# Kernel optimization log

Measured on AMD Instinct MI355X. Metric: run time of the kernel, lower is better.

## Reference

```python
import jax, jax.numpy as jnp
import numpy as np

BETA = 0.25
NUM_EMBEDS = 1024
EMBED_DIM = 256


def setup_inputs() -> dict:
    key = jax.random.key(0)
    k1, k2 = jax.random.split(key)
    z_e = jax.random.normal(k1, (32, EMBED_DIM, 1024), dtype=jnp.float32)
    lim = 1.0 / NUM_EMBEDS
    embed_weight = jax.random.uniform(k2, (NUM_EMBEDS, EMBED_DIM), dtype=jnp.float32,
                                      minval=-lim, maxval=lim)
    return {"z_e": z_e, "embed_weight": embed_weight}


def reference(z_e, embed_weight):
    # z_e: (b, d, t) -> (b, t, d)
    ze = jnp.transpose(z_e, (0, 2, 1))
    b, t, d = ze.shape
    flat = ze.reshape(-1, d)  # (N, d)
    K = embed_weight.shape[0]
    # squared euclidean distances (N, K) via sum-of-squares + matmul
    distances = (jnp.sum(flat ** 2, axis=1, keepdims=True)
                 + jnp.sum(embed_weight ** 2, axis=1)
                 - 2.0 * flat @ embed_weight.T)
    idx = jnp.argmin(distances, axis=1)  # (N,)
    # one-hot @ W is just a gather
    z_q = embed_weight[idx].reshape(b, t, d)
    # commitment / codebook losses (mse over all elements)
    e_latent_loss = jnp.mean((jax.lax.stop_gradient(z_q) - ze) ** 2)
    q_latent_loss = jnp.mean((z_q - jax.lax.stop_gradient(ze)) ** 2)
    reg_loss = q_latent_loss + BETA * e_latent_loss
    # straight-through estimator
    z_q_st = ze + jax.lax.stop_gradient(z_q - ze)
    z_q_out = jnp.transpose(z_q_st, (0, 2, 1))  # (b, d, t)
    # perplexity from codebook usage
    N = flat.shape[0]
    avg_probs = jnp.zeros((K,), dtype=jnp.float32).at[idx].add(1.0) / N
    perplexity = jnp.exp(-jnp.sum(avg_probs * jnp.log(avg_probs + 1e-10)))
    return (z_q_out, reg_loss, perplexity)
```

## Files before the change

kernel.cpp:

```cpp
#include <hip/hip_runtime.h>
#include <math.h>

#define BB 32
#define DD 256
#define TT 1024
#define KK 1024
#define NN (BB*TT)

#define BROWS 64
#define CCH   256
#define DSL   64
#define NSTEP 16


__global__ void prep_kernel(const float* __restrict__ W, float* __restrict__ wsq,
                            int* __restrict__ counts, float* __restrict__ sse) {
    const int k = blockIdx.x;
    const int lane = threadIdx.x;
    const float4 v = ((const float4*)(W + (size_t)k * DD))[lane];
    double s = (double)v.x * v.x + (double)v.y * v.y + (double)v.z * v.z + (double)v.w * v.w;
    #pragma unroll
    for (int m = 32; m > 0; m >>= 1) s += __shfl_down(s, m);
    if (lane == 0) wsq[k] = (float)s;
    if (blockIdx.x < 16) counts[blockIdx.x * 64 + lane] = 0;
    if (blockIdx.x == 0 && lane == 0) *sse = 0.0f;
}

__device__ __forceinline__ int swz_w(int r, int q) { return r * 16 + (q ^ ((r >> 3) & 7)); }
__device__ __forceinline__ int swz_z(int r, int q) { return r * 16 + (q ^ (r & 7) ^ ((r >> 3) & 7)); }

__device__ __forceinline__ void gl_lds16(const float* g, void* l) {
    __builtin_amdgcn_global_load_lds((const __attribute__((address_space(1))) void*)g,
                                     (__attribute__((address_space(3))) void*)l, 16, 0, 0);
}

__global__ __launch_bounds__(256, 2) void vq_fused_kernel(
    const float* __restrict__ z, const float* __restrict__ W,
    const float* __restrict__ wsq, float* __restrict__ out,
    int* __restrict__ counts, float* __restrict__ sse)
{
    __shared__ float4 zs[BROWS * 16];
    __shared__ float4 ws[CCH * 16];
    const int tid = threadIdx.x;
    const int tx = tid & 31, ty = tid >> 5;
    const int w = tid >> 6, lane = tid & 63;
    const int row0 = blockIdx.x * BROWS;
    const int b = row0 >> 10, t0 = row0 & 1023;
    const size_t bbase = (size_t)b * DD * TT;
    const float* zbase = z + bbase + t0;

    float rsq[8];
    {
        const int ro = lane & 15;
        const int g  = lane >> 4;
        const float* zp = zbase + (size_t)g * 64 * TT + (16 * w + ro);
        double s = 0.0;
        #pragma unroll 4
        for (int d = 0; d < 64; ++d) { float v = zp[(size_t)d * TT]; s += (double)v * v; }
        s += __shfl_xor(s, 16);
        s += __shfl_xor(s, 32);
        float f = (float)s;
        #pragma unroll
        for (int i = 0; i < 8; ++i) rsq[i] = __shfl(f, (ty & 1) * 8 + i);
    }

    float minv[8]; int mini[8];
    #pragma unroll
    for (int i = 0; i < 8; ++i) { minv[i] = 3.4e38f; mini[i] = 0; }

    const int zr = tid & 63;
    const int zq0 = w * 4;
    float4 zreg[4];
    {
        #pragma unroll
        for (int j = 0; j < 4; ++j) {
            const float* zp = zbase + (size_t)((zq0 + j) * 4) * TT + zr;
            zreg[j].x = zp[0]; zreg[j].y = zp[(size_t)TT];
            zreg[j].z = zp[(size_t)2 * TT]; zreg[j].w = zp[(size_t)3 * TT];
        }
    }

    const int wr0 = w * 64 + (lane >> 4);
    const int wslot = lane & 15;
    char* const wlbase = (char*)ws + (size_t)w * 16384;

    float acc[8][8];
    float wq[8];

    for (int s = 0; s < NSTEP; ++s) {
        const int sl = s & 3, ch = s >> 2;
        __syncthreads();
        #pragma unroll
        for (int j = 0; j < 4; ++j) zs[swz_z(zr, zq0 + j)] = zreg[j];
        {
            const float* wch = W + (size_t)(ch * CCH) * DD + sl * DSL;
            #pragma unroll
            for (int k = 0; k < 16; ++k) {
                int r = wr0 + k * 4;
                const float* g = wch + (size_t)r * DD + 4 * (wslot ^ ((r >> 3) & 7));
                gl_lds16(g, wlbase + k * 1024);
            }
        }
        __syncthreads();

        if (sl == 0) {
            #pragma unroll
            for (int i = 0; i < 8; ++i)
                #pragma unroll
                for (int j = 0; j < 8; ++j) acc[i][j] = 0.0f;
            #pragma unroll
            for (int j = 0; j < 8; ++j) wq[j] = wsq[ch * CCH + tx * 8 + j];
        }
        if (s < NSTEP - 1) {
            const int sln = (s + 1) & 3;
            #pragma unroll
            for (int j = 0; j < 4; ++j) {
                const float* zp = zbase + (size_t)(sln * DSL + (zq0 + j) * 4) * TT + zr;
                zreg[j].x = zp[0]; zreg[j].y = zp[(size_t)TT];
                zreg[j].z = zp[(size_t)2 * TT]; zreg[j].w = zp[(size_t)3 * TT];
            }
        }
        for (int q = 0; q < 16; ++q) {
            float4 zf[8], wf[8];
            #pragma unroll
            for (int i = 0; i < 8; ++i) zf[i] = zs[swz_z(ty * 8 + i, q)];
            #pragma unroll
            for (int j = 0; j < 8; ++j) wf[j] = ws[swz_w(tx * 8 + j, q)];
            #pragma unroll
            for (int i = 0; i < 8; ++i)
                #pragma unroll
                for (int j = 0; j < 8; ++j) {
                    acc[i][j] = fmaf(zf[i].x, wf[j].x, acc[i][j]);
                    acc[i][j] = fmaf(zf[i].y, wf[j].y, acc[i][j]);
                    acc[i][j] = fmaf(zf[i].z, wf[j].z, acc[i][j]);
                    acc[i][j] = fmaf(zf[i].w, wf[j].w, acc[i][j]);
                }
        }
        if (sl == 3) {
            #pragma unroll
            for (int j = 0; j < 8; ++j) {
                int c = ch * CCH + tx * 8 + j;
                #pragma unroll
                for (int i = 0; i < 8; ++i) {
                    float s1 = rsq[i] + wq[j];
                    float v = fmaf(-2.0f, acc[i][j], s1);
                    if (v < minv[i]) { minv[i] = v; mini[i] = c; }
                }
            }
        }
    }

    __syncthreads();
    int* idxs = (int*)zs;
    float* ssescr = (float*)zs + 64;
    #pragma unroll
    for (int i = 0; i < 8; ++i) {
        float v = minv[i]; int ix = mini[i];
        #pragma unroll
        for (int m = 1; m < 32; m <<= 1) {
            float ov = __shfl_xor(v, m);
            int   oi = __shfl_xor(ix, m);
            if (ov < v || (ov == v && oi < ix)) { v = ov; ix = oi; }
        }
        if (tx == 0) {
            idxs[ty * 8 + i] = ix;
            atomicAdd(&counts[ix], 1);
        }
    }
    __syncthreads();

    const int tg = tid & 15;
    const int dg = tid >> 4;
    const int t4 = tg * 4;
    int ixs[4];
    #pragma unroll
    for (int m = 0; m < 4; ++m) ixs[m] = idxs[t4 + m];
    float ssel = 0.0f;
    #pragma unroll
    for (int k4 = 0; k4 < 4; ++k4) {
        const int d0 = dg * 16 + k4 * 4;
        float wr[4][4];
        #pragma unroll
        for (int m = 0; m < 4; ++m) {
            float4 wv = *(const float4*)(W + (size_t)ixs[m] * DD + d0);
            wr[m][0] = wv.x; wr[m][1] = wv.y; wr[m][2] = wv.z; wr[m][3] = wv.w;
        }
        #pragma unroll
        for (int dd = 0; dd < 4; ++dd) {
            const int d = d0 + dd;
            const size_t base = bbase + (size_t)d * TT + t0 + t4;
            float4 zv = *(const float4*)(z + base);
            float e0 = wr[0][dd] - zv.x, e1 = wr[1][dd] - zv.y;
            float e2 = wr[2][dd] - zv.z, e3 = wr[3][dd] - zv.w;
            float4 o;
            o.x = zv.x + e0; o.y = zv.y + e1; o.z = zv.z + e2; o.w = zv.w + e3;
            *(float4*)(out + base) = o;
            ssel += (e0 * e0 + e1 * e1) + (e2 * e2 + e3 * e3);
        }
    }
    #pragma unroll
    for (int m = 32; m > 0; m >>= 1) ssel += __shfl_down(ssel, m);
    if (lane == 0) ssescr[w] = ssel;
    __syncthreads();
    if (tid == 0) atomicAdd(sse, (ssescr[0] + ssescr[1]) + (ssescr[2] + ssescr[3]));
}

__global__ void finalize_kernel(const int* __restrict__ counts, const float* __restrict__ sse,
                                float* __restrict__ out) {
    float s = 0.0f;
    for (int k = threadIdx.x; k < KK; k += 256) {
        float p = (float)counts[k] / (float)NN;
        s += p * logf(p + 1e-10f);
    }
    #pragma unroll
    for (int m = 32; m > 0; m >>= 1) s += __shfl_down(s, m);
    __shared__ float wsum[4];
    if ((threadIdx.x & 63) == 0) wsum[threadIdx.x >> 6] = s;
    __syncthreads();
    if (threadIdx.x == 0) {
        float ent = (wsum[0] + wsum[1]) + (wsum[2] + wsum[3]);
        out[(size_t)BB * DD * TT]     = 1.25f * (*sse) / (float)(BB * DD * TT);
        out[(size_t)BB * DD * TT + 1] = expf(-ent);
    }
}

extern "C" void kernel_launch(void* const* d_in, const int* in_sizes, int n_in,
                              void* d_out, int out_size, void* d_ws, size_t ws_size,
                              hipStream_t stream) {
    const float* z = (const float*)d_in[0];
    const float* W = (const float*)d_in[1];
    float* out = (float*)d_out;

    float* wsq    = (float*)d_ws;
    int*   counts = (int*)(wsq + 1024);
    float* sse    = (float*)(counts + 1024);

    prep_kernel<<<1024, 64, 0, stream>>>(W, wsq, counts, sse);
    vq_fused_kernel<<<NN / BROWS, 256, 0, stream>>>(z, W, wsq, out, counts, sse);
    finalize_kernel<<<1, 256, 0, stream>>>(counts, sse, out);
}
```

Before: 272.2 us.

## Double-buffer LDS tiles with one barrier per step and a narrower K slice

Splits the shared-memory z and W tiles into two buffers. The next step's tiles (W via global_load_lds, z from registers) are staged while the current buffer is being computed, so each step needs one barrier instead of two. The K slice per step shrinks from 64 to 32 dims (32 steps instead of 16), which keeps total LDS the same. The inner q loop is now fully unrolled. This is meant to hide global-to-LDS latency behind the FMA work, at the cost of twice as many barriers across steps, larger code, and more register pressure.

```diff
diff --git a/kernel.cpp b/kernel.cpp
--- a/kernel.cpp
+++ b/kernel.cpp
@@ -9,8 +9,8 @@
 
 #define BROWS 64
 #define CCH   256
-#define DSL   64
-#define NSTEP 16
+#define DSL   32
+#define NSTEP 32
 
 
 __global__ void prep_kernel(const float* __restrict__ W, float* __restrict__ wsq,
@@ -26,8 +26,8 @@
     if (blockIdx.x == 0 && lane == 0) *sse = 0.0f;
 }
 
-__device__ __forceinline__ int swz_w(int r, int q) { return r * 16 + (q ^ ((r >> 3) & 7)); }
-__device__ __forceinline__ int swz_z(int r, int q) { return r * 16 + (q ^ (r & 7) ^ ((r >> 3) & 7)); }
+__device__ __forceinline__ int swz_w(int r, int q) { return r * 8 + (q ^ ((r >> 3) & 7)); }
+__device__ __forceinline__ int swz_z(int r, int q) { return r * 8 + (q ^ (r & 7) ^ ((r >> 3) & 7)); }
 
 __device__ __forceinline__ void gl_lds16(const float* g, void* l) {
     __builtin_amdgcn_global_load_lds((const __attribute__((address_space(1))) void*)g,
@@ -39,8 +39,8 @@
     const float* __restrict__ wsq, float* __restrict__ out,
     int* __restrict__ counts, float* __restrict__ sse)
 {
-    __shared__ float4 zs[BROWS * 16];
-    __shared__ float4 ws[CCH * 16];
+    __shared__ float4 zs[2][BROWS * 8];
+    __shared__ float4 ws[2][CCH * 8];
     const int tid = threadIdx.x;
     const int tx = tid & 31, ty = tid >> 5;
     const int w = tid >> 6, lane = tid & 63;
@@ -68,41 +68,53 @@
     #pragma unroll
     for (int i = 0; i < 8; ++i) { minv[i] = 3.4e38f; mini[i] = 0; }
 
-    const int zr = tid & 63;
-    const int zq0 = w * 4;
-    float4 zreg[4];
-    {
-        #pragma unroll
-        for (int j = 0; j < 4; ++j) {
-            const float* zp = zbase + (size_t)((zq0 + j) * 4) * TT + zr;
+    const int zr  = lane;
+    const int zq0 = w * 2;
+    const int wlr = lane >> 3;
+    const int wls = lane & 7;
+    float4 zreg[2];
+
+    auto STAGE_W = [&](int t) {
+        const int ch = t >> 3, sl = t & 7;
+        const float* wch = W + (size_t)(ch * CCH) * DD + sl * DSL;
+        char* dst = (char*)&ws[t & 1][0] + (size_t)w * 8192;
+        #pragma unroll
+        for (int k = 0; k < 8; ++k) {
+            const int r = w * 64 + k * 8 + wlr;
+            const float* g = wch + (size_t)r * DD + 4 * (wls ^ k);
+            gl_lds16(g, dst + k * 1024);
+        }
+    };
+    auto LOAD_Z = [&](int t) {
+        const int sl = t & 7;
+        #pragma unroll
+        for (int j = 0; j < 2; ++j) {
+            const float* zp = zbase + (size_t)(sl * DSL + (zq0 + j) * 4) * TT + zr;
             zreg[j].x = zp[0]; zreg[j].y = zp[(size_t)TT];
             zreg[j].z = zp[(size_t)2 * TT]; zreg[j].w = zp[(size_t)3 * TT];
         }
-    }
-
-    const int wr0 = w * 64 + (lane >> 4);
-    const int wslot = lane & 15;
-    char* const wlbase = (char*)ws + (size_t)w * 16384;
+    };
+    auto WRITE_Z = [&](int t) {
+        #pragma unroll
+        for (int j = 0; j < 2; ++j) zs[t & 1][swz_z(zr, zq0 + j)] = zreg[j];
+    };
+
+    LOAD_Z(0);
+    STAGE_W(0);
+    WRITE_Z(0);
+    LOAD_Z(1);
 
     float acc[8][8];
     float wq[8];
 
     for (int s = 0; s < NSTEP; ++s) {
-        const int sl = s & 3, ch = s >> 2;
+        const int sl = s & 7, ch = s >> 3;
         __syncthreads();
-        #pragma unroll
-        for (int j = 0; j < 4; ++j) zs[swz_z(zr, zq0 + j)] = zreg[j];
-        {
-            const float* wch = W + (size_t)(ch * CCH) * DD + sl * DSL;
-            #pragma unroll
-            for (int k = 0; k < 16; ++k) {
-                int r = wr0 + k * 4;
-                const float* g = wch + (size_t)r * DD + 4 * (wslot ^ ((r >> 3) & 7));
-                gl_lds16(g, wlbase + k * 1024);
-            }
-        }
-        __syncthreads();
-
+        if (s + 1 < NSTEP) {
+            STAGE_W(s + 1);
+            WRITE_Z(s + 1);
+            if (s + 2 < NSTEP) LOAD_Z(s + 2);
+        }
         if (sl == 0) {
             #pragma unroll
             for (int i = 0; i < 8; ++i)
@@ -111,21 +123,13 @@
             #pragma unroll
             for (int j = 0; j < 8; ++j) wq[j] = wsq[ch * CCH + tx * 8 + j];
         }
-        if (s < NSTEP - 1) {
-            const int sln = (s + 1) & 3;
-            #pragma unroll
-            for (int j = 0; j < 4; ++j) {
-                const float* zp = zbase + (size_t)(sln * DSL + (zq0 + j) * 4) * TT + zr;
-                zreg[j].x = zp[0]; zreg[j].y = zp[(size_t)TT];
-                zreg[j].z = zp[(size_t)2 * TT]; zreg[j].w = zp[(size_t)3 * TT];
-            }
-        }
-        for (int q = 0; q < 16; ++q) {
+        #pragma unroll
+        for (int q = 0; q < 8; ++q) {
             float4 zf[8], wf[8];
             #pragma unroll
-            for (int i = 0; i < 8; ++i) zf[i] = zs[swz_z(ty * 8 + i, q)];
-            #pragma unroll
-            for (int j = 0; j < 8; ++j) wf[j] = ws[swz_w(tx * 8 + j, q)];
+            for (int i = 0; i < 8; ++i) zf[i] = zs[s & 1][swz_z(ty * 8 + i, q)];
+            #pragma unroll
+            for (int j = 0; j < 8; ++j) wf[j] = ws[s & 1][swz_w(tx * 8 + j, q)];
             #pragma unroll
             for (int i = 0; i < 8; ++i)
                 #pragma unroll
@@ -136,7 +140,7 @@
                     acc[i][j] = fmaf(zf[i].w, wf[j].w, acc[i][j]);
                 }
         }
-        if (sl == 3) {
+        if (sl == 7) {
             #pragma unroll
             for (int j = 0; j < 8; ++j) {
                 int c = ch * CCH + tx * 8 + j;
@@ -151,8 +155,8 @@
     }
 
     __syncthreads();
-    int* idxs = (int*)zs;
-    float* ssescr = (float*)zs + 64;
+    int* idxs = (int*)&zs[0][0];
+    float* ssescr = (float*)&zs[0][0] + 64;
     #pragma unroll
     for (int i = 0; i < 8; ++i) {
         float v = minv[i]; int ix = mini[i];
```

Measured after the change: 408.3 us. 1.5x slower.

## Double-buffer codebook tiles in LDS with async prefetch of next slice

Applied to the files above, without the earlier changes.

The codebook LDS tile is split into two half-size buffers (32-wide d-slices) so the global-to-LDS load for the next step is issued before computing on the current one. The z tile is still written once per 64-wide slice and consumed over two steps. This is meant to hide W load latency behind the FMA loop instead of stalling on a barrier after each load. The cost is twice as many steps and barriers, with LDS size unchanged.

```diff
diff --git a/kernel.cpp b/kernel.cpp
--- a/kernel.cpp
+++ b/kernel.cpp
@@ -9,8 +9,8 @@
 
 #define BROWS 64
 #define CCH   256
-#define DSL   64
-#define NSTEP 16
+#define WSL   32
+#define NSTEP 32
 
 
 __global__ void prep_kernel(const float* __restrict__ W, float* __restrict__ wsq,
@@ -26,8 +26,8 @@
     if (blockIdx.x == 0 && lane == 0) *sse = 0.0f;
 }
 
-__device__ __forceinline__ int swz_w(int r, int q) { return r * 16 + (q ^ ((r >> 3) & 7)); }
 __device__ __forceinline__ int swz_z(int r, int q) { return r * 16 + (q ^ (r & 7) ^ ((r >> 3) & 7)); }
+__device__ __forceinline__ int swz_w(int r, int q) { return r * 8 + (q ^ ((r >> 3) & 7)); }
 
 __device__ __forceinline__ void gl_lds16(const float* g, void* l) {
     __builtin_amdgcn_global_load_lds((const __attribute__((address_space(1))) void*)g,
@@ -40,7 +40,7 @@
     int* __restrict__ counts, float* __restrict__ sse)
 {
     __shared__ float4 zs[BROWS * 16];
-    __shared__ float4 ws[CCH * 16];
+    __shared__ float4 ws[2][CCH * 8];
     const int tid = threadIdx.x;
     const int tx = tid & 31, ty = tid >> 5;
     const int w = tid >> 6, lane = tid & 63;
@@ -48,6 +48,28 @@
     const int b = row0 >> 10, t0 = row0 & 1023;
     const size_t bbase = (size_t)b * DD * TT;
     const float* zbase = z + bbase + t0;
+
+    const int zr  = lane;
+    const int zq0 = w * 4;
+    const int wlr = lane >> 3;
+    const int wls = lane & 7;
+    float4 zreg[4];
+
+    {
+        const float* wch = W;
+        char* dst = (char*)&ws[0][0] + (size_t)w * 8192;
+        #pragma unroll
+        for (int k = 0; k < 8; ++k) {
+            const int r = w * 64 + k * 8 + wlr;
+            gl_lds16(wch + (size_t)r * DD + 4 * (wls ^ k), dst + k * 1024);
+        }
+        #pragma unroll
+        for (int j = 0; j < 4; ++j) {
+            const float* zp = zbase + (size_t)((zq0 + j) * 4) * TT + zr;
+            zreg[j].x = zp[0]; zreg[j].y = zp[(size_t)TT];
+            zreg[j].z = zp[(size_t)2 * TT]; zreg[j].w = zp[(size_t)3 * TT];
+        }
+    }
 
     float rsq[8];
     {
@@ -68,41 +90,36 @@
     #pragma unroll
     for (int i = 0; i < 8; ++i) { minv[i] = 3.4e38f; mini[i] = 0; }
 
-    const int zr = tid & 63;
-    const int zq0 = w * 4;
-    float4 zreg[4];
-    {
-        #pragma unroll
-        for (int j = 0; j < 4; ++j) {
-            const float* zp = zbase + (size_t)((zq0 + j) * 4) * TT + zr;
-            zreg[j].x = zp[0]; zreg[j].y = zp[(size_t)TT];
-            zreg[j].z = zp[(size_t)2 * TT]; zreg[j].w = zp[(size_t)3 * TT];
-        }
-    }
-
-    const int wr0 = w * 64 + (lane >> 4);
-    const int wslot = lane & 15;
-    char* const wlbase = (char*)ws + (size_t)w * 16384;
-
     float acc[8][8];
     float wq[8];
 
     for (int s = 0; s < NSTEP; ++s) {
-        const int sl = s & 3, ch = s >> 2;
+        const int h = s & 1, sl = s & 7, ch = s >> 3;
         __syncthreads();
-        #pragma unroll
-        for (int j = 0; j < 4; ++j) zs[swz_z(zr, zq0 + j)] = zreg[j];
-        {
-            const float* wch = W + (size_t)(ch * CCH) * DD + sl * DSL;
-            #pragma unroll
-            for (int k = 0; k < 16; ++k) {
-                int r = wr0 + k * 4;
-                const float* g = wch + (size_t)r * DD + 4 * (wslot ^ ((r >> 3) & 7));
-                gl_lds16(g, wlbase + k * 1024);
+        if (h == 0) {
+            #pragma unroll
+            for (int j = 0; j < 4; ++j) zs[swz_z(zr, zq0 + j)] = zreg[j];
+            __syncthreads();
+        }
+        if (s + 1 < NSTEP) {
+            const int t = s + 1, sln = t & 7, chn = t >> 3;
+            const float* wch = W + (size_t)(chn * CCH) * DD + sln * WSL;
+            char* dst = (char*)&ws[t & 1][0] + (size_t)w * 8192;
+            #pragma unroll
+            for (int k = 0; k < 8; ++k) {
+                const int r = w * 64 + k * 8 + wlr;
+                gl_lds16(wch + (size_t)r * DD + 4 * (wls ^ k), dst + k * 1024);
             }
         }
-        __syncthreads();
-
+        if (h == 0 && s + 2 < NSTEP) {
+            const int mn = ((s + 2) & 7) >> 1;
+            #pragma unroll
+            for (int j = 0; j < 4; ++j) {
+                const float* zp = zbase + (size_t)(mn * 64 + (zq0 + j) * 4) * TT + zr;
+                zreg[j].x = zp[0]; zreg[j].y = zp[(size_t)TT];
+                zreg[j].z = zp[(size_t)2 * TT]; zreg[j].w = zp[(size_t)3 * TT];
+            }
+        }
         if (sl == 0) {
             #pragma unroll
             for (int i = 0; i < 8; ++i)
@@ -111,21 +128,13 @@
             #pragma unroll
             for (int j = 0; j < 8; ++j) wq[j] = wsq[ch * CCH + tx * 8 + j];
         }
-        if (s < NSTEP - 1) {
-            const int sln = (s + 1) & 3;
-            #pragma unroll
-            for (int j = 0; j < 4; ++j) {
-                const float* zp = zbase + (size_t)(sln * DSL + (zq0 + j) * 4) * TT + zr;
-                zreg[j].x = zp[0]; zreg[j].y = zp[(size_t)TT];
-                zreg[j].z = zp[(size_t)2 * TT]; zreg[j].w = zp[(size_t)3 * TT];
-            }
-        }
-        for (int q = 0; q < 16; ++q) {
+        const int qb = 8 * h;
+        for (int q = 0; q < 8; ++q) {
             float4 zf[8], wf[8];
             #pragma unroll
-            for (int i = 0; i < 8; ++i) zf[i] = zs[swz_z(ty * 8 + i, q)];
-            #pragma unroll
-            for (int j = 0; j < 8; ++j) wf[j] = ws[swz_w(tx * 8 + j, q)];
+            for (int i = 0; i < 8; ++i) zf[i] = zs[swz_z(ty * 8 + i, qb + q)];
+            #pragma unroll
+            for (int j = 0; j < 8; ++j) wf[j] = ws[h][swz_w(tx * 8 + j, q)];
             #pragma unroll
             for (int i = 0; i < 8; ++i)
                 #pragma unroll
@@ -136,7 +145,7 @@
                     acc[i][j] = fmaf(zf[i].w, wf[j].w, acc[i][j]);
                 }
         }
-        if (sl == 3) {
+        if (sl == 7) {
             #pragma unroll
             for (int j = 0; j < 8; ++j) {
                 int c = ch * CCH + tx * 8 + j;
@@ -151,8 +160,8 @@
     }
 
     __syncthreads();
-    int* idxs = (int*)zs;
-    float* ssescr = (float*)zs + 64;
+    int* idxs = (int*)&zs[0];
+    float* ssescr = (float*)&zs[0] + 64;
     #pragma unroll
     for (int i = 0; i < 8; ++i) {
         float v = minv[i]; int ix = mini[i];
```

Measured after the change: 278.6 us. 1.02x slower.

## Restructure distance GEMM: one row per lane, per-wave codebook slices double-buffered

Applied to the files above, without the earlier changes.

Reorganizes the distance computation so each lane owns one z row and each wave scans its own 256-code slice of the codebook in 64-code chunks, accumulating 64 partial dot products per lane. The codebook tiles are streamed into per-wave double-buffered LDS with async global-to-LDS loads, and z is staged less often. The argmin is then reduced across waves through LDS instead of cross-lane shuffles. This removes most block-wide barriers on W loads, but gives up the 8x8 register outer-product reuse, so LDS reads per FMA rise (W reads are wave-uniform broadcasts). It also adds a 64-float accumulator array that raises register pressure.

```diff
diff --git a/kernel.cpp b/kernel.cpp
--- a/kernel.cpp
+++ b/kernel.cpp
@@ -8,9 +8,7 @@
 #define NN (BB*TT)
 
 #define BROWS 64
-#define CCH   256
-#define DSL   64
-#define NSTEP 16
+#define NSTEP 32
 
 
 __global__ void prep_kernel(const float* __restrict__ W, float* __restrict__ wsq,
@@ -26,9 +24,6 @@
     if (blockIdx.x == 0 && lane == 0) *sse = 0.0f;
 }
 
-__device__ __forceinline__ int swz_w(int r, int q) { return r * 16 + (q ^ ((r >> 3) & 7)); }
-__device__ __forceinline__ int swz_z(int r, int q) { return r * 16 + (q ^ (r & 7) ^ ((r >> 3) & 7)); }
-
 __device__ __forceinline__ void gl_lds16(const float* g, void* l) {
     __builtin_amdgcn_global_load_lds((const __attribute__((address_space(1))) void*)g,
                                      (__attribute__((address_space(3))) void*)l, 16, 0, 0);
@@ -40,16 +35,33 @@
     int* __restrict__ counts, float* __restrict__ sse)
 {
     __shared__ float4 zs[BROWS * 16];
-    __shared__ float4 ws[CCH * 16];
+    __shared__ float4 wsl[4][2][64 * 8];
     const int tid = threadIdx.x;
-    const int tx = tid & 31, ty = tid >> 5;
     const int w = tid >> 6, lane = tid & 63;
     const int row0 = blockIdx.x * BROWS;
     const int b = row0 >> 10, t0 = row0 & 1023;
     const size_t bbase = (size_t)b * DD * TT;
     const float* zbase = z + bbase + t0;
 
-    float rsq[8];
+    const int zq0 = w * 4;
+    float4 zreg[4];
+
+    {
+        const int cb = w * 256;
+        char* dst = (char*)&wsl[w][0][0];
+        #pragma unroll
+        for (int k = 0; k < 8; ++k)
+            gl_lds16(W + (size_t)(cb + k * 8 + (lane >> 3)) * DD + (lane & 7) * 4,
+                     dst + k * 1024);
+        #pragma unroll
+        for (int j = 0; j < 4; ++j) {
+            const float* zp = zbase + (size_t)((zq0 + j) * 4) * TT + lane;
+            zreg[j].x = zp[0]; zreg[j].y = zp[(size_t)TT];
+            zreg[j].z = zp[(size_t)2 * TT]; zreg[j].w = zp[(size_t)3 * TT];
+        }
+    }
+
+    float rsq;
     {
         const int ro = lane & 15;
         const int g  = lane >> 4;
@@ -60,112 +72,93 @@
         s += __shfl_xor(s, 16);
         s += __shfl_xor(s, 32);
         float f = (float)s;
-        #pragma unroll
-        for (int i = 0; i < 8; ++i) rsq[i] = __shfl(f, (ty & 1) * 8 + i);
-    }
-
-    float minv[8]; int mini[8];
-    #pragma unroll
-    for (int i = 0; i < 8; ++i) { minv[i] = 3.4e38f; mini[i] = 0; }
-
-    const int zr = tid & 63;
-    const int zq0 = w * 4;
-    float4 zreg[4];
-    {
-        #pragma unroll
-        for (int j = 0; j < 4; ++j) {
-            const float* zp = zbase + (size_t)((zq0 + j) * 4) * TT + zr;
-            zreg[j].x = zp[0]; zreg[j].y = zp[(size_t)TT];
-            zreg[j].z = zp[(size_t)2 * TT]; zreg[j].w = zp[(size_t)3 * TT];
-        }
-    }
-
-    const int wr0 = w * 64 + (lane >> 4);
-    const int wslot = lane & 15;
-    char* const wlbase = (char*)ws + (size_t)w * 16384;
-
-    float acc[8][8];
-    float wq[8];
-
-    for (int s = 0; s < NSTEP; ++s) {
-        const int sl = s & 3, ch = s >> 2;
         __syncthreads();
-        #pragma unroll
-        for (int j = 0; j < 4; ++j) zs[swz_z(zr, zq0 + j)] = zreg[j];
-        {
-            const float* wch = W + (size_t)(ch * CCH) * DD + sl * DSL;
-            #pragma unroll
-            for (int k = 0; k < 16; ++k) {
-                int r = wr0 + k * 4;
-                const float* g = wch + (size_t)r * DD + 4 * (wslot ^ ((r >> 3) & 7));
-                gl_lds16(g, wlbase + k * 1024);
-            }
-        }
+        if (lane < 16) ((float*)zs)[16 * w + lane] = f;
         __syncthreads();
-
-        if (sl == 0) {
-            #pragma unroll
-            for (int i = 0; i < 8; ++i)
+        rsq = ((float*)zs)[lane];
+        __syncthreads();
+    }
+
+    float minv = 3.4e38f; int mini = 0;
+    float acc[64];
+
+    for (int t = 0; t < NSTEP; ++t) {
+        const int c = t >> 3, dd = t & 7, h = t & 1;
+        if (h == 0) {
+            __syncthreads();
+            #pragma unroll
+            for (int j = 0; j < 4; ++j)
+                zs[(lane << 4) | ((zq0 + j) ^ (lane & 7))] = zreg[j];
+            __syncthreads();
+            if (t + 2 < NSTEP) {
+                const int d0n = ((t + 2) & 7) * 32;
                 #pragma unroll
-                for (int j = 0; j < 8; ++j) acc[i][j] = 0.0f;
-            #pragma unroll
-            for (int j = 0; j < 8; ++j) wq[j] = wsq[ch * CCH + tx * 8 + j];
-        }
-        if (s < NSTEP - 1) {
-            const int sln = (s + 1) & 3;
-            #pragma unroll
-            for (int j = 0; j < 4; ++j) {
-                const float* zp = zbase + (size_t)(sln * DSL + (zq0 + j) * 4) * TT + zr;
-                zreg[j].x = zp[0]; zreg[j].y = zp[(size_t)TT];
-                zreg[j].z = zp[(size_t)2 * TT]; zreg[j].w = zp[(size_t)3 * TT];
-            }
-        }
-        for (int q = 0; q < 16; ++q) {
-            float4 zf[8], wf[8];
-            #pragma unroll
-            for (int i = 0; i < 8; ++i) zf[i] = zs[swz_z(ty * 8 + i, q)];
-            #pragma unroll
-            for (int j = 0; j < 8; ++j) wf[j] = ws[swz_w(tx * 8 + j, q)];
-            #pragma unroll
-            for (int i = 0; i < 8; ++i)
-                #pragma unroll
-                for (int j = 0; j < 8; ++j) {
-                    acc[i][j] = fmaf(zf[i].x, wf[j].x, acc[i][j]);
-                    acc[i][j] = fmaf(zf[i].y, wf[j].y, acc[i][j]);
-                    acc[i][j] = fmaf(zf[i].z, wf[j].z, acc[i][j]);
-                    acc[i][j] = fmaf(zf[i].w, wf[j].w, acc[i][j]);
-                }
-        }
-        if (sl == 3) {
-            #pragma unroll
-            for (int j = 0; j < 8; ++j) {
-                int c = ch * CCH + tx * 8 + j;
-                #pragma unroll
-                for (int i = 0; i < 8; ++i) {
-                    float s1 = rsq[i] + wq[j];
-                    float v = fmaf(-2.0f, acc[i][j], s1);
-                    if (v < minv[i]) { minv[i] = v; mini[i] = c; }
+                for (int j = 0; j < 4; ++j) {
+                    const float* zp = zbase + (size_t)(d0n + (zq0 + j) * 4) * TT + lane;
+                    zreg[j].x = zp[0]; zreg[j].y = zp[(size_t)TT];
+                    zreg[j].z = zp[(size_t)2 * TT]; zreg[j].w = zp[(size_t)3 * TT];
                 }
             }
         }
-    }
-
-    __syncthreads();
-    int* idxs = (int*)zs;
-    float* ssescr = (float*)zs + 64;
-    #pragma unroll
-    for (int i = 0; i < 8; ++i) {
-        float v = minv[i]; int ix = mini[i];
-        #pragma unroll
-        for (int m = 1; m < 32; m <<= 1) {
-            float ov = __shfl_xor(v, m);
-            int   oi = __shfl_xor(ix, m);
-            if (ov < v || (ov == v && oi < ix)) { v = ov; ix = oi; }
-        }
-        if (tx == 0) {
-            idxs[ty * 8 + i] = ix;
-            atomicAdd(&counts[ix], 1);
-        }
+        asm volatile("s_waitcnt vmcnt(0)" ::: "memory");
+        if (t + 1 < NSTEP) {
+            const int tn = t + 1;
+            const int cbn = w * 256 + (tn >> 3) * 64, d0n = (tn & 7) * 32;
+            char* dst = (char*)&wsl[w][tn & 1][0];
+            #pragma unroll
+            for (int k = 0; k < 8; ++k)
+                gl_lds16(W + (size_t)(cbn + k * 8 + (lane >> 3)) * DD + d0n + (lane & 7) * 4,
+                         dst + k * 1024);
+        }
+        if (dd == 0) {
+            #pragma unroll
+            for (int j = 0; j < 64; ++j) acc[j] = 0.0f;
+        }
+        const float4* wb = &wsl[w][h][0];
+        #pragma clang loop unroll(disable)
+        for (int dq = 0; dq < 8; ++dq) {
+            const int dqg = (h << 3) | dq;
+            float4 z4 = zs[(lane << 4) | (dqg ^ (lane & 7))];
+            const float4* wp = wb + dq;
+            #pragma unroll
+            for (int j = 0; j < 64; ++j) {
+                float4 wf = wp[j * 8];
+                acc[j] = fmaf(z4.x, wf.x, acc[j]);
+                acc[j] = fmaf(z4.y, wf.y, acc[j]);
+                acc[j] = fmaf(z4.z, wf.z, acc[j]);
+                acc[j] = fmaf(z4.w, wf.w, acc[j]);
+            }
+        }
+        if (dd == 7) {
+            const int cb = w * 256 + c * 64;
+            const float* wqp = wsq + cb;
+            #pragma unroll
+            for (int j = 0; j < 64; ++j) {
+                float s1 = rsq + wqp[j];
+                float v = fmaf(-2.0f, acc[j], s1);
+                if (v < minv) { minv = v; mini = cb + j; }
+            }
+        }
+    }
+
+    __syncthreads();
+    float* cand_v = (float*)zs;
+    int*   cand_i = (int*)zs + 256;
+    int*   idxs   = (int*)zs + 512;
+    float* ssescr = (float*)zs + 640;
+    cand_v[w * 64 + lane] = minv;
+    cand_i[w * 64 + lane] = mini;
+    __syncthreads();
+    if (tid < 64) {
+        float bv = cand_v[tid]; int bi = cand_i[tid];
+        #pragma unroll
+        for (int ww = 1; ww < 4; ++ww) {
+            float v = cand_v[ww * 64 + tid];
+            int  ii = cand_i[ww * 64 + tid];
+            if (v < bv) { bv = v; bi = ii; }
+        }
+        idxs[tid] = bi;
+        atomicAdd(&counts[bi], 1);
     }
     __syncthreads();
 
```

Measured after the change: 465.0 us. 70.8% more time.
